# Kernel tuning notes

Hardware: AMD Instinct MI355X
Metric: run time of the kernel (lower is better)

The kernel has to match this reference:

```python
import jax, jax.numpy as jnp
import numpy as np

B, S, D_MODEL, H, BLOCK = 2, 4096, 1024, 16, 512
HEAD = D_MODEL // H  # 64


def setup_inputs() -> dict:
    key = jax.random.key(0)
    ks = jax.random.split(key, 5)
    w_scale = 1.0 / np.sqrt(D_MODEL)  # variance_scaling(1.0,'fan_in','normal')-like magnitude
    return {
        "inputs_q": jax.random.normal(ks[0], (B, S, D_MODEL), jnp.float32),
        "Wq": jax.random.normal(ks[1], (D_MODEL, D_MODEL), jnp.float32) * w_scale,
        "bq": jnp.zeros((D_MODEL,), jnp.float32),
        "Wk": jax.random.normal(ks[2], (D_MODEL, D_MODEL), jnp.float32) * w_scale,
        "bk": jnp.zeros((D_MODEL,), jnp.float32),
        "Wv": jax.random.normal(ks[3], (D_MODEL, D_MODEL), jnp.float32) * w_scale,
        "bv": jnp.zeros((D_MODEL,), jnp.float32),
        "Wo": jax.random.normal(ks[4], (D_MODEL, D_MODEL), jnp.float32) * w_scale,
        "bo": jnp.zeros((D_MODEL,), jnp.float32),
    }


def _flash_attention(q, k, v):
    """Blocked online-softmax attention. q,k,v: [B,S,H,D] -> [B,S,H,D].

    Scans over KV blocks of size BLOCK, maintaining running max (m),
    running sum of exp (l), and unnormalized output (o), exactly matching
    the original module's blocked accumulation math (no mask/bias/dropout).
    """
    scale = 1.0 / jnp.sqrt(jnp.asarray(HEAD, q.dtype))
    n_kv_blocks = S // BLOCK
    # [n_blocks, B, BLOCK, H, D]
    kb = k.reshape(B, n_kv_blocks, BLOCK, H, HEAD).transpose(1, 0, 2, 3, 4)
    vb = v.reshape(B, n_kv_blocks, BLOCK, H, HEAD).transpose(1, 0, 2, 3, 4)

    o0 = jnp.zeros_like(q)                                   # [B,S,H,D]
    m0 = jnp.full((B, S, H), -jnp.inf, dtype=q.dtype)        # running max
    l0 = jnp.zeros((B, S, H), dtype=q.dtype)                 # running sum-exp

    def step(carry, kv):
        o, m, l = carry
        k_blk, v_blk = kv
        # [B,H,S,BLOCK] scores for all queries vs this kv block
        scores = jnp.einsum('bqhd,bkhd->bhqk', q, k_blk) * scale
        blk_max = jnp.max(scores, axis=-1).transpose(0, 2, 1)   # [B,S,H]
        new_m = jnp.maximum(m, blk_max)
        alpha = jnp.exp(m - new_m)                               # rescale old stats
        p = jnp.exp(scores - new_m.transpose(0, 2, 1)[..., None])
        new_l = alpha * l + jnp.sum(p, axis=-1).transpose(0, 2, 1)
        new_o = o * alpha[..., None] + jnp.einsum('bhqk,bkhd->bqhd', p, v_blk)
        return (new_o, new_m, new_l), None

    (o, m, l), _ = jax.lax.scan(step, (o0, m0, l0), (kb, vb))
    return o / l[..., None]


def reference(inputs_q, Wq, bq, Wk, bk, Wv, bv, Wo, bo):
    q = (inputs_q @ Wq + bq).reshape(B, S, H, HEAD)
    k = (inputs_q @ Wk + bk).reshape(B, S, H, HEAD)  # self-attention: k=v=q input
    v = (inputs_q @ Wv + bv).reshape(B, S, H, HEAD)
    x = _flash_attention(q, k, v).reshape(B, S, D_MODEL)
    return x @ Wo + bo
```

## Files before the change

kernel.cpp:

```cpp
#include <hip/hip_runtime.h>
#include <hip/hip_bf16.h>
#include <stdint.h>

#define B_ 2
#define S_ 4096
#define DM 1024
#define H_ 16
#define HD 64
#define M_TOT (B_*S_)

typedef unsigned short u16;
typedef short s16x8 __attribute__((ext_vector_type(8)));
typedef short s16x4 __attribute__((ext_vector_type(4)));
typedef float f32x4 __attribute__((ext_vector_type(4)));
typedef uint32_t u32x2 __attribute__((ext_vector_type(2)));

#if __has_builtin(__builtin_amdgcn_mfma_f32_16x16x16_bf16)
#define MFMA16(A,B,C) __builtin_amdgcn_mfma_f32_16x16x16_bf16(A,B,C,0,0,0)
#elif __has_builtin(__builtin_amdgcn_mfma_f32_16x16x16bf16_1k)
#define MFMA16(A,B,C) __builtin_amdgcn_mfma_f32_16x16x16bf16_1k(A,B,C,0,0,0)
#else
static __device__ __forceinline__ f32x4 mfma16_asm(s16x4 a, s16x4 b, f32x4 c){
  f32x4 d;
  asm volatile("v_mfma_f32_16x16x16_bf16 %0, %1, %2, %3" : "=v"(d) : "v"(a), "v"(b), "v"(c));
  return d;
}
#define MFMA16(A,B,C) mfma16_asm(A,B,C)
#endif

__device__ __forceinline__ u16 f2bf(float f){
  union { float fv; uint32_t u; } x; x.fv = f;
  uint32_t r = (x.u + 0x7fffu + ((x.u >> 16) & 1u)) >> 16;
  return (u16)r;
}

#if __has_builtin(__builtin_amdgcn_cvt_pk_bf16_f32)
typedef __bf16 bf16x2_t __attribute__((ext_vector_type(2)));
__device__ __forceinline__ uint32_t pkbf(float a, float b){
  union { bf16x2_t v; uint32_t u; } x;
  x.v = __builtin_amdgcn_cvt_pk_bf16_f32(a, b);
  return x.u;
}
#else
__device__ __forceinline__ uint32_t pkbf(float a, float b){
  union { float f; uint32_t u; } xa, xb; xa.f = a; xb.f = b;
  return __builtin_amdgcn_perm(xb.u + 0x8000u, xa.u + 0x8000u, 0x07060302u);
}
#endif

__device__ __forceinline__ void gld_lds16(const void* g, void* l){
  __builtin_amdgcn_global_load_lds((const __attribute__((address_space(1))) void*)g,
                                   (__attribute__((address_space(3))) void*)l, 16, 0, 0);
}

__global__ __launch_bounds__(256) void k_cvt_x(const float* __restrict__ x, u16* __restrict__ xb){
  size_t i = (size_t)blockIdx.x * 256 + threadIdx.x;
  const float4* p = (const float4*)x + i*2;
  float4 a = p[0], b = p[1];
  union { u16 u[8]; uint4 v; } o;
  o.u[0]=f2bf(a.x); o.u[1]=f2bf(a.y); o.u[2]=f2bf(a.z); o.u[3]=f2bf(a.w);
  o.u[4]=f2bf(b.x); o.u[5]=f2bf(b.y); o.u[6]=f2bf(b.z); o.u[7]=f2bf(b.w);
  ((uint4*)xb)[i] = o.v;
}

__global__ __launch_bounds__(256) void k_wt(const float* __restrict__ W0, const float* __restrict__ W1,
                                            const float* __restrict__ W2, const float* __restrict__ W3,
                                            u16* __restrict__ wt){
  const float* W = blockIdx.z==0?W0: blockIdx.z==1?W1: blockIdx.z==2?W2:W3;
  u16* out = wt + (size_t)blockIdx.z * DM * DM;
  int n0 = blockIdx.x*64, k0 = blockIdx.y*64;
  __shared__ u16 T[64*66];
  int t = threadIdx.x;
  #pragma unroll
  for (int i=0;i<4;i++){
    int idx = t + i*256;
    int kr = idx >> 4, n4 = idx & 15;
    float4 v = *(const float4*)(W + (size_t)(k0+kr)*DM + n0 + n4*4);
    T[(n4*4+0)*66 + kr] = f2bf(v.x);
    T[(n4*4+1)*66 + kr] = f2bf(v.y);
    T[(n4*4+2)*66 + kr] = f2bf(v.z);
    T[(n4*4+3)*66 + kr] = f2bf(v.w);
  }
  __syncthreads();
  #pragma unroll
  for (int i=0;i<2;i++){
    int idx = t + i*256;
    int n = idx >> 3, k8 = idx & 7;
    union { u16 u[8]; uint4 v; } o;
    #pragma unroll
    for (int j=0;j<8;j++) o.u[j] = T[n*66 + k8*8 + j];
    *(uint4*)(out + (size_t)(n0+n)*DM + k0 + k8*8) = o.v;
  }
}

__device__ __forceinline__ void gemm128(const u16* __restrict__ A, const u16* __restrict__ BT,
                                        const float* __restrict__ bias, float scale,
                                        u16* __restrict__ outb, float* __restrict__ outf,
                                        int m0, int n0){
  __shared__ __align__(16) u16 As[128*32];
  __shared__ __align__(16) u16 Bs[128*32];
  int t = threadIdx.x;
  int lane = t & 63, w = t >> 6;
  int wm = w & 1, wn = w >> 1;
  int c16 = lane & 15, quad = lane >> 4;
  f32x4 acc[4][4] = {};
  for (int k0 = 0; k0 < DM; k0 += 32){
    #pragma unroll
    for (int i=0;i<2;i++){
      int idx = t + i*256;
      int row = idx >> 2, c8 = (idx & 3) << 3;
      gld_lds16(A  + (size_t)(m0+row)*DM + k0 + c8, &As[idx*8]);
      gld_lds16(BT + (size_t)(n0+row)*DM + k0 + c8, &Bs[idx*8]);
    }
    __syncthreads();
    s16x8 af[4], bf[4];
    #pragma unroll
    for (int mi=0;mi<4;mi++) af[mi] = *(const s16x8*)&As[(wm*64+mi*16+c16)*32 + quad*8];
    #pragma unroll
    for (int ni=0;ni<4;ni++) bf[ni] = *(const s16x8*)&Bs[(wn*64+ni*16+c16)*32 + quad*8];
    #pragma unroll
    for (int mi=0;mi<4;mi++)
      #pragma unroll
      for (int ni=0;ni<4;ni++)
        acc[mi][ni] = __builtin_amdgcn_mfma_f32_16x16x32_bf16(af[mi], bf[ni], acc[mi][ni], 0, 0, 0);
    __syncthreads();
  }
  #pragma unroll
  for (int mi=0;mi<4;mi++){
    #pragma unroll
    for (int ni=0;ni<4;ni++){
      int col = n0 + wn*64 + ni*16 + c16;
      float bc = bias[col];
      #pragma unroll
      for (int r=0;r<4;r++){
        int row = m0 + wm*64 + mi*16 + quad*4 + r;
        float v = (acc[mi][ni][r] + bc) * scale;
        if (outb) outb[(size_t)row*DM + col] = f2bf(v);
        else      outf[(size_t)row*DM + col] = v;
      }
    }
  }
}

#define CL2 0.18033688011112042f

__global__ __launch_bounds__(256) void k_gemm_qkv(const u16* __restrict__ xb, const u16* __restrict__ wt,
                                                  const float* __restrict__ b0, const float* __restrict__ b1,
                                                  const float* __restrict__ b2,
                                                  u16* __restrict__ q, u16* __restrict__ k, u16* __restrict__ v){
  int z = blockIdx.z;
  const u16* BT = wt + (size_t)z*DM*DM;
  const float* bias = z==0?b0: z==1?b1:b2;
  u16* out = z==0?q: z==1?k:v;
  float scale = (z==0) ? CL2 : 1.0f;
  gemm128(xb, BT, bias, scale, out, nullptr, blockIdx.y*128, blockIdx.x*128);
}

__global__ __launch_bounds__(256) void k_gemm_out(const u16* __restrict__ ab, const u16* __restrict__ wto,
                                                  const float* __restrict__ bias, float* __restrict__ out){
  gemm128(ab, wto, bias, 1.0f, nullptr, out, blockIdx.y*128, blockIdx.x*128);
}

__global__ __launch_bounds__(256) void k_vt(const u16* __restrict__ vb, u16* __restrict__ vt){
  __shared__ u16 T[64*66];
  int s0 = blockIdx.x*64, h = blockIdx.y, b = blockIdx.z;
  int t = threadIdx.x;
  #pragma unroll
  for (int i=0;i<2;i++){
    int idx = t + i*256;
    int sr = idx >> 3, d8 = idx & 7;
    s16x8 v = *(const s16x8*)(vb + ((size_t)(b*S_ + s0 + sr))*DM + h*64 + d8*8);
    #pragma unroll
    for (int j=0;j<8;j++) T[(d8*8+j)*66 + sr] = ((const u16*)&v)[j];
  }
  __syncthreads();
  #pragma unroll
  for (int i=0;i<2;i++){
    int idx = t + i*256;
    int d = idx >> 3, s8 = idx & 7;
    union { u16 u[8]; uint4 v; } o;
    #pragma unroll
    for (int j=0;j<8;j++) o.u[j] = T[d*66 + s8*8 + j];
    *(uint4*)(vt + ((size_t)((b*H_ + h)*64 + d))*S_ + s0 + s8*8) = o.v;
  }
}

__global__ __launch_bounds__(512, 2) void k_attn(const u16* __restrict__ qg, const u16* __restrict__ kg,
                                                 const u16* __restrict__ vtg, u16* __restrict__ ao){
  __shared__ __align__(16) char smem[38912];
  u16*   Kb  = (u16*)smem;
  u16*   Vb  = (u16*)(smem + 18432);
  float* Ob  = (float*)smem;
  u16*   ObT = (u16*)smem;
  float* Lb  = (float*)(smem + 36864);

  int t = threadIdx.x, lane = t & 63, w = t >> 6;
  int c16 = lane & 15, quad = lane >> 4;
  int qq = w & 3, kh = w >> 2;
  int h = blockIdx.y, b = blockIdx.z;
  int q0 = blockIdx.x * 256;
  size_t rowbase = (size_t)b * S_;
  const u16* vbase = vtg + ((size_t)(b*H_ + h)) * 64 * S_;

  s16x8 qf[4][2];
  #pragma unroll
  for (int nt=0;nt<4;nt++)
    #pragma unroll
    for (int ks=0;ks<2;ks++)
      qf[nt][ks] = *(const s16x8*)(qg + (rowbase + q0 + qq*64 + nt*16 + c16)*DM + h*64 + ks*32 + quad*8);

  f32x4 oacc[4][4] = {};
  float lacc[4] = {0.f,0.f,0.f,0.f};

  for (int kv0 = 0; kv0 < S_; kv0 += 128){
    __syncthreads();
    #pragma unroll
    for (int i=0;i<2;i++){
      int idx = t + i*512;
      int kr = idx >> 3, kc = (idx & 7)*8;
      *(s16x8*)&Kb[kr*72 + kc] = *(const s16x8*)(kg + (rowbase + kv0 + kr)*DM + h*64 + kc);
      int vd = idx >> 4, vc = (idx & 15)*8;
      *(s16x8*)&Vb[vd*136 + vc] = *(const s16x8*)(vbase + (size_t)vd*S_ + kv0 + vc);
    }
    __syncthreads();

    f32x4 sc[4][4] = {};
    #pragma unroll
    for (int mt=0;mt<4;mt++){
      #pragma unroll
      for (int ks=0;ks<2;ks++){
        s16x8 kf = *(const s16x8*)&Kb[(kh*64 + mt*16 + c16)*72 + ks*32 + quad*8];
        #pragma unroll
        for (int nt=0;nt<4;nt++)
          sc[mt][nt] = __builtin_amdgcn_mfma_f32_16x16x32_bf16(kf, qf[nt][ks], sc[mt][nt], 0,0,0);
      }
    }

    uint32_t pk[4][4][2];
    #pragma unroll
    for (int mt=0;mt<4;mt++){
      #pragma unroll
      for (int nt=0;nt<4;nt++){
        float p0 = __builtin_amdgcn_exp2f(sc[mt][nt][0]);
        float p1 = __builtin_amdgcn_exp2f(sc[mt][nt][1]);
        float p2 = __builtin_amdgcn_exp2f(sc[mt][nt][2]);
        float p3 = __builtin_amdgcn_exp2f(sc[mt][nt][3]);
        lacc[nt] += (p0 + p1) + (p2 + p3);
        pk[mt][nt][0] = pkbf(p0, p1);
        pk[mt][nt][1] = pkbf(p2, p3);
      }
    }

    #pragma unroll
    for (int mt=0;mt<4;mt++){
      #pragma unroll
      for (int dt=0;dt<4;dt++){
        s16x4 vf = *(const s16x4*)&Vb[(dt*16 + c16)*136 + kh*64 + mt*16 + quad*4];
        #pragma unroll
        for (int nt=0;nt<4;nt++){
          union { uint32_t u[2]; s16x4 v; } pp;
          pp.u[0] = pk[mt][nt][0]; pp.u[1] = pk[mt][nt][1];
          oacc[dt][nt] = MFMA16(vf, pp.v, oacc[dt][nt]);
        }
      }
    }
  }

  float lw[4];
  #pragma unroll
  for (int nt=0;nt<4;nt++){
    float l = lacc[nt];
    l += __shfl_xor(l, 16);
    l += __shfl_xor(l, 32);
    lw[nt] = l;
  }
  __syncthreads();
  if (quad == 0){
    #pragma unroll
    for (int nt=0;nt<4;nt++) Lb[kh*256 + qq*64 + nt*16 + c16] = lw[nt];
  }
  uint32_t pko[4][4][2];
  float invl[4];
  #pragma unroll
  for (int dh=0; dh<2; dh++){
    if (kh == 1){
      #pragma unroll
      for (int dt2=0;dt2<2;dt2++)
        #pragma unroll
        for (int nt=0;nt<4;nt++)
          *(f32x4*)&Ob[(qq*64 + nt*16 + c16)*36 + dt2*16 + quad*4] = oacc[dh*2+dt2][nt];
    }
    __syncthreads();
    if (kh == 0){
      if (dh == 0){
        #pragma unroll
        for (int nt=0;nt<4;nt++){
          int ql = qq*64 + nt*16 + c16;
          invl[nt] = 1.0f / (Lb[ql] + Lb[256 + ql]);
        }
      }
      #pragma unroll
      for (int dt2=0;dt2<2;dt2++)
        #pragma unroll
        for (int nt=0;nt<4;nt++){
          f32x4 p = *(const f32x4*)&Ob[(qq*64 + nt*16 + c16)*36 + dt2*16 + quad*4];
          f32x4 o = oacc[dh*2+dt2][nt] + p;
          pko[dh*2+dt2][nt][0] = pkbf(o[0]*invl[nt], o[1]*invl[nt]);
          pko[dh*2+dt2][nt][1] = pkbf(o[2]*invl[nt], o[3]*invl[nt]);
        }
    }
    __syncthreads();
  }
  if (kh == 0){
    #pragma unroll
    for (int dt=0;dt<4;dt++)
      #pragma unroll
      for (int nt=0;nt<4;nt++){
        u32x2 pr; pr.x = pko[dt][nt][0]; pr.y = pko[dt][nt][1];
        *(u32x2*)&ObT[(qq*64 + nt*16 + c16)*72 + dt*16 + quad*4] = pr;
      }
  }
  __syncthreads();
  #pragma unroll
  for (int i=0;i<4;i++){
    int idx = t + i*512;
    int qr = idx >> 3, qc = (idx & 7)*8;
    *(s16x8*)(ao + (rowbase + q0 + qr)*DM + h*64 + qc) = *(const s16x8*)&ObT[qr*72 + qc];
  }
}

extern "C" void kernel_launch(void* const* d_in, const int* in_sizes, int n_in,
                              void* d_out, int out_size, void* d_ws, size_t ws_size,
                              hipStream_t stream){
  const float* x  = (const float*)d_in[0];
  const float* Wq = (const float*)d_in[1];
  const float* bq = (const float*)d_in[2];
  const float* Wk = (const float*)d_in[3];
  const float* bk = (const float*)d_in[4];
  const float* Wv = (const float*)d_in[5];
  const float* bv = (const float*)d_in[6];
  const float* Wo = (const float*)d_in[7];
  const float* bo = (const float*)d_in[8];

  char* ws = (char*)d_ws;
  const size_t XB = (size_t)M_TOT*DM*2;
  const size_t WTB = (size_t)4*DM*DM*2;
  u16* xb  = (u16*)(ws);
  u16* wt  = (u16*)(ws + XB);
  u16* qb  = (u16*)(ws + XB + WTB);
  u16* kb  = (u16*)(ws + XB + WTB + XB);
  u16* vb  = (u16*)(ws + XB + WTB + 2*XB);
  u16* vtb = (u16*)(ws + XB + WTB + 3*XB);
  u16* aob = (u16*)(ws + XB + WTB + 4*XB);

  k_cvt_x<<<dim3((M_TOT*DM)/(256*8)), 256, 0, stream>>>(x, xb);
  k_wt<<<dim3(16,16,4), 256, 0, stream>>>(Wq, Wk, Wv, Wo, wt);
  k_gemm_qkv<<<dim3(8, M_TOT/128, 3), 256, 0, stream>>>(xb, wt, bq, bk, bv, qb, kb, vb);
  k_vt<<<dim3(S_/64, H_, B_), 256, 0, stream>>>(vb, vtb);
  k_attn<<<dim3(S_/256, H_, B_), 512, 0, stream>>>(qb, kb, vtb, aob);
  k_gemm_out<<<dim3(8, M_TOT/128), 256, 0, stream>>>(aob, wt + (size_t)3*DM*DM, bo, (float*)d_out);
}
```

Baseline: 382.0 us.

## Double-buffer K/V tiles with direct global-to-LDS loads and XOR swizzle

```diff
diff --git a/kernel.cpp b/kernel.cpp
--- a/kernel.cpp
+++ b/kernel.cpp
@@ -187,12 +187,10 @@
 
 __global__ __launch_bounds__(512, 2) void k_attn(const u16* __restrict__ qg, const u16* __restrict__ kg,
                                                  const u16* __restrict__ vtg, u16* __restrict__ ao){
-  __shared__ __align__(16) char smem[38912];
-  u16*   Kb  = (u16*)smem;
-  u16*   Vb  = (u16*)(smem + 18432);
+  __shared__ __align__(16) char smem[67584];
   float* Ob  = (float*)smem;
   u16*   ObT = (u16*)smem;
-  float* Lb  = (float*)(smem + 36864);
+  float* Lb  = (float*)(smem + 65536);
 
   int t = threadIdx.x, lane = t & 63, w = t >> 6;
   int c16 = lane & 15, quad = lane >> 4;
@@ -202,6 +200,29 @@
   size_t rowbase = (size_t)b * S_;
   const u16* vbase = vtg + ((size_t)(b*H_ + h)) * 64 * S_;
 
+  int krow0 = t >> 3,         ksw0 = ((t & 7) ^ (krow0 & 7));
+  int krow1 = (t + 512) >> 3, ksw1 = ((t & 7) ^ (krow1 & 7));
+  const u16* kgp0 = kg + (rowbase + krow0)*DM + h*64 + ksw0*8;
+  const u16* kgp1 = kg + (rowbase + krow1)*DM + h*64 + ksw1*8;
+  int vrow0 = t >> 4,         vsw0 = ((t & 15) ^ (vrow0 & 15));
+  int vrow1 = (t + 512) >> 4, vsw1 = ((t & 15) ^ (vrow1 & 15));
+  const u16* vgp0 = vbase + (size_t)vrow0*S_ + vsw0*8;
+  const u16* vgp1 = vbase + (size_t)vrow1*S_ + vsw1*8;
+  char* kd0 = smem + t*16;
+  char* kd1 = smem + t*16 + 8192;
+  char* vd0 = smem + 16384 + t*16;
+  char* vd1 = smem + 16384 + t*16 + 8192;
+
+  auto stage = [&](int boff, int kv0){
+    size_t ko = (size_t)kv0 * DM;
+    gld_lds16(kgp0 + ko, kd0 + boff);
+    gld_lds16(kgp1 + ko, kd1 + boff);
+    gld_lds16(vgp0 + kv0, vd0 + boff);
+    gld_lds16(vgp1 + kv0, vd1 + boff);
+  };
+
+  stage(0, 0);
+
   s16x8 qf[4][2];
   #pragma unroll
   for (int nt=0;nt<4;nt++)
@@ -212,24 +233,16 @@
   f32x4 oacc[4][4] = {};
   float lacc[4] = {0.f,0.f,0.f,0.f};
 
-  for (int kv0 = 0; kv0 < S_; kv0 += 128){
-    __syncthreads();
-    #pragma unroll
-    for (int i=0;i<2;i++){
-      int idx = t + i*512;
-      int kr = idx >> 3, kc = (idx & 7)*8;
-      *(s16x8*)&Kb[kr*72 + kc] = *(const s16x8*)(kg + (rowbase + kv0 + kr)*DM + h*64 + kc);
-      int vd = idx >> 4, vc = (idx & 15)*8;
-      *(s16x8*)&Vb[vd*136 + vc] = *(const s16x8*)(vbase + (size_t)vd*S_ + kv0 + vc);
-    }
-    __syncthreads();
+  auto compute = [&](int boff){
+    const u16* Kt = (const u16*)(smem + boff);
+    const u16* Vt = (const u16*)(smem + boff + 16384);
 
     f32x4 sc[4][4] = {};
     #pragma unroll
     for (int mt=0;mt<4;mt++){
       #pragma unroll
       for (int ks=0;ks<2;ks++){
-        s16x8 kf = *(const s16x8*)&Kb[(kh*64 + mt*16 + c16)*72 + ks*32 + quad*8];
+        s16x8 kf = *(const s16x8*)&Kt[(kh*64 + mt*16 + c16)*64 + (((ks*4 + quad) ^ (c16 & 7)) * 8)];
         #pragma unroll
         for (int nt=0;nt<4;nt++)
           sc[mt][nt] = __builtin_amdgcn_mfma_f32_16x16x32_bf16(kf, qf[nt][ks], sc[mt][nt], 0,0,0);
@@ -255,7 +268,7 @@
     for (int mt=0;mt<4;mt++){
       #pragma unroll
       for (int dt=0;dt<4;dt++){
-        s16x4 vf = *(const s16x4*)&Vb[(dt*16 + c16)*136 + kh*64 + mt*16 + quad*4];
+        s16x4 vf = *(const s16x4*)&Vt[(dt*16 + c16)*128 + (((kh*8 + mt*2 + (quad>>1)) ^ c16) * 8) + (quad & 1)*4];
         #pragma unroll
         for (int nt=0;nt<4;nt++){
           union { uint32_t u[2]; s16x4 v; } pp;
@@ -264,7 +277,23 @@
         }
       }
     }
-  }
+  };
+
+  #define NT (S_/128)
+  #pragma unroll 1
+  for (int kvt = 0; kvt < NT-1; ++kvt){
+    stage(((kvt+1) & 1) * 32768, (kvt+1)*128);
+    asm volatile("s_waitcnt vmcnt(4)" ::: "memory");
+    __builtin_amdgcn_s_barrier();
+    __builtin_amdgcn_sched_barrier(0);
+    compute((kvt & 1) * 32768);
+    __builtin_amdgcn_s_barrier();
+    __builtin_amdgcn_sched_barrier(0);
+  }
+  asm volatile("s_waitcnt vmcnt(0)" ::: "memory");
+  __builtin_amdgcn_s_barrier();
+  __builtin_amdgcn_sched_barrier(0);
+  compute(((NT-1) & 1) * 32768);
 
   float lw[4];
   #pragma unroll
```

New measurement: 355.7 us. 1.07x faster.
